# Kernel tuning notes

Hardware: AMD Instinct MI355X
Metric: run time of the kernel (lower is better)

The kernel has to match this reference:

```python
import jax, jax.numpy as jnp
import numpy as np

HID = 128


def _mlp(f, W1, b1, W2, b2, W3, b3):
    h = jax.nn.relu(f @ W1 + b1)
    h = jax.nn.relu(h @ W2 + b2)
    return h @ W3 + b3


def setup_inputs() -> dict:
    key = jax.random.key(0)
    ks = jax.random.split(key, 20)
    B, T = 4096, 256
    x = jax.random.normal(ks[0], (B, T + 1, 2), dtype=jnp.float32)
    t = jax.random.uniform(ks[1], (B, 1), dtype=jnp.float32)

    def lin(k, fan_in, fan_out):
        return jax.random.normal(k, (fan_in, fan_out), jnp.float32) / jnp.sqrt(jnp.float32(fan_in))

    inp = {"x": x, "t": t}
    # forward_score MLP: input = [x_i(2), t(1), x_prev(2), n(1), path_t(2)] = 8
    inp["fw_W1"], inp["fw_b1"] = lin(ks[2], 8, HID), jnp.zeros((HID,), jnp.float32)
    inp["fw_W2"], inp["fw_b2"] = lin(ks[3], HID, HID), jnp.zeros((HID,), jnp.float32)
    inp["fw_W3"], inp["fw_b3"] = lin(ks[4], HID, 2), jnp.zeros((2,), jnp.float32)
    # backward_score MLP: input = [x_i(2), t(1), x_next(2), n(1), path_t(2)] = 8
    inp["bw_W1"], inp["bw_b1"] = lin(ks[5], 8, HID), jnp.zeros((HID,), jnp.float32)
    inp["bw_W2"], inp["bw_b2"] = lin(ks[6], HID, HID), jnp.zeros((HID,), jnp.float32)
    inp["bw_W3"], inp["bw_b3"] = lin(ks[7], HID, 2), jnp.zeros((2,), jnp.float32)
    # initial_score MLP: input = [x_0(2), t(1)] = 3
    inp["in_W1"], inp["in_b1"] = lin(ks[8], 3, HID), jnp.zeros((HID,), jnp.float32)
    inp["in_W2"], inp["in_b2"] = lin(ks[9], HID, HID), jnp.zeros((HID,), jnp.float32)
    inp["in_W3"], inp["in_b3"] = lin(ks[10], HID, 2), jnp.zeros((2,), jnp.float32)
    return inp


def reference(x, t,
              fw_W1, fw_b1, fw_W2, fw_b2, fw_W3, fw_b3,
              bw_W1, bw_b1, bw_W2, bw_b2, bw_W3, bw_b3,
              in_W1, in_b1, in_W2, in_b2, in_W3, in_b3):
    # x: [B, T+1, 2]; last slot is path_t. Equivalent of NeuralNet.get_score,
    # with the per-timestep Python loop batched across the time dimension.
    B = x.shape[0]
    T = x.shape[1] - 1  # ts_len
    x_n = x[:, :-1]                     # [B, T, 2]
    path_t = x[:, -1]                   # [B, 2]

    t_b = jnp.broadcast_to(t[:, None, :], (B, T - 1, 1))        # [B, T-1, 1]
    pt_b = jnp.broadcast_to(path_t[:, None, :], (B, T - 1, 2))  # [B, T-1, 2]

    # forward_score applied at i = 1..T-1, neighbor = x[:, i-1], n = i/T
    n_fwd = (jnp.arange(1, T, dtype=jnp.float32) / T)[None, :, None]
    n_fwd = jnp.broadcast_to(n_fwd, (B, T - 1, 1))
    fwd_feat = jnp.concatenate([x_n[:, 1:], t_b, x_n[:, :-1], n_fwd, pt_b], axis=-1)  # [B,T-1,8]
    fwd_out = _mlp(fwd_feat, fw_W1, fw_b1, fw_W2, fw_b2, fw_W3, fw_b3)                # [B,T-1,2]

    # backward_score applied at i = 0..T-2, neighbor = x[:, i+1], n = i/T
    n_bwd = (jnp.arange(0, T - 1, dtype=jnp.float32) / T)[None, :, None]
    n_bwd = jnp.broadcast_to(n_bwd, (B, T - 1, 1))
    bwd_feat = jnp.concatenate([x_n[:, :-1], t_b, x_n[:, 1:], n_bwd, pt_b], axis=-1)  # [B,T-1,8]
    bwd_out = _mlp(bwd_feat, bw_W1, bw_b1, bw_W2, bw_b2, bw_W3, bw_b3)                # [B,T-1,2]

    # initial_score at i = 0
    init_feat = jnp.concatenate([x_n[:, 0], t], axis=-1)                               # [B,3]
    init_out = _mlp(init_feat, in_W1, in_b1, in_W2, in_b2, in_W3, in_b3)               # [B,2]

    score = jnp.zeros((B, T, 2), dtype=x.dtype)
    score = score.at[:, 1:].add(fwd_out)
    score = score.at[:, :T - 1].add(bwd_out)
    score = score.at[:, 0].add(init_out)
    return score
```

## Files before the change

### kernel.cpp

```cpp
#include <hip/hip_runtime.h>
#include <stdint.h>

typedef __attribute__((ext_vector_type(8))) short short8;
typedef __attribute__((ext_vector_type(4))) float floatx4;

#define MFMA16(a, b, c) __builtin_amdgcn_mfma_f32_16x16x32_bf16(a, b, c, 0, 0, 0)

__device__ __forceinline__ unsigned pkbf(float lo, float hi) {
    const unsigned a = __builtin_bit_cast(unsigned, lo) + 0x8000u;
    const unsigned b = __builtin_bit_cast(unsigned, hi) + 0x8000u;
    return __builtin_amdgcn_perm(b, a, 0x07060302u);
}
__device__ __forceinline__ unsigned short f2bf(float x) {
    unsigned u = __builtin_bit_cast(unsigned, x);
    u = (u + 0x7fffu + ((u >> 16) & 1u)) >> 16;
    return (unsigned short)u;
}

__device__ __forceinline__ int hphys(int row, int u) {
    return row * 64 + ((((u >> 2) ^ (row & 15)) << 2) | (u & 3));
}

__global__ __launch_bounds__(256)
__attribute__((amdgpu_waves_per_eu(4, 4)))
void NeuralNet_37615323578557_kernel(
        const float* __restrict__ x, const float* __restrict__ t,
        const float* __restrict__ fW1, const float* __restrict__ fb1,
        const float* __restrict__ fW2, const float* __restrict__ fb2,
        const float* __restrict__ fW3, const float* __restrict__ fb3,
        const float* __restrict__ gW1, const float* __restrict__ gb1,
        const float* __restrict__ gW2, const float* __restrict__ gb2,
        const float* __restrict__ gW3, const float* __restrict__ gb3,
        const float* __restrict__ iW1, const float* __restrict__ ib1,
        const float* __restrict__ iW2, const float* __restrict__ ib2,
        const float* __restrict__ iW3, const float* __restrict__ ib3,
        float* __restrict__ out) {
    __shared__ unsigned sbuf[8192];
    __shared__ unsigned short fbuf[64 * 8];
    __shared__ float accT[2 * 256 * 2];
    __shared__ unsigned short w3img[256];

    unsigned* const h1buf = sbuf;
    unsigned* const h2buf = sbuf + 4096;

    const int tid  = threadIdx.x;
    const int lane = tid & 63;
    const int w    = tid >> 6;
    const int c    = lane & 15;
    const int q    = lane >> 4;
    const int b0   = blockIdx.x * 2;

    #pragma unroll
    for (int k = 0; k < 4; ++k) accT[tid + k * 256] = 0.0f;
    __syncthreads();

    if (w < 2) {
        float* h1s = (float*)fbuf + w * 128;
        const int b = b0 + w;
        const float* xb = x + (size_t)b * 514;
        const float f0 = xb[0], f1 = xb[1], f2 = t[b];
        const int u0 = lane, u1 = lane + 64;
        const float h0 = fmaxf(iW1[u0] * f0 + iW1[128 + u0] * f1 + iW1[256 + u0] * f2 + ib1[u0], 0.f);
        const float h1 = fmaxf(iW1[u1] * f0 + iW1[128 + u1] * f1 + iW1[256 + u1] * f2 + ib1[u1], 0.f);
        h1s[u0] = h0;
        h1s[u1] = h1;
        float a0 = ib2[lane], a1 = ib2[lane + 64];
        for (int k = 0; k < 128; ++k) {
            const float hv = h1s[k];
            a0 += hv * iW2[k * 128 + lane];
            a1 += hv * iW2[k * 128 + lane + 64];
        }
        a0 = fmaxf(a0, 0.f); a1 = fmaxf(a1, 0.f);
        float p0 = a0 * iW3[lane * 2 + 0] + a1 * iW3[(lane + 64) * 2 + 0];
        float p1 = a0 * iW3[lane * 2 + 1] + a1 * iW3[(lane + 64) * 2 + 1];
        #pragma unroll
        for (int m = 1; m < 64; m <<= 1) {
            p0 += __shfl_xor(p0, m, 64);
            p1 += __shfl_xor(p1, m, 64);
        }
        if (lane == 0) {
            accT[w * 512 + 0] += p0 + ib3[0];
            accT[w * 512 + 1] += p1 + ib3[1];
        }
    }

    const int wbase = w * 32;
    const int ucol  = w * 16 + c;

    for (int dir = 0; dir < 2; ++dir) {
        const float* W1 = dir ? gW1 : fW1;
        const float* B1 = dir ? gb1 : fb1;
        const float* W2 = dir ? gW2 : fW2;
        const float* B2 = dir ? gb2 : fb2;
        const float* W3 = dir ? gW3 : fW3;
        const float* B3 = dir ? gb3 : fb3;
        const int posoff = (1 - dir) * 2;

        __syncthreads();

        {
            const int k0  = (tid & 63) << 1;
            const int c0  = (tid >> 6) << 5;
            const int rot = (tid >> 2) & 15;
            const int ks  = k0 >> 5;
            const int q2  = (k0 >> 3) & 3;
            const int j0  = k0 & 7;
            const float* r0p = &W2[k0 * 128 + c0];
            const float* r1p = r0p + 128;
            const int usb = (q2 << 4) * 8 + j0;
            #pragma unroll 4
            for (int nn2 = 0; nn2 < 16; ++nn2) {
                const int off = ((nn2 + rot) & 15) << 1;
                const float2 v0 = *(const float2*)(r0p + off);
                const float2 v1 = *(const float2*)(r1p + off);
                #pragma unroll
                for (int e = 0; e < 2; ++e) {
                    const int n = c0 + off + e;
                    const unsigned pv = pkbf(e ? v0.y : v0.x, e ? v1.y : v1.x);
                    const int B = ((n >> 5) * 2 + (n & 1)) * 4 + ks;
                    const int us = B * 512 + ((n >> 1) & 15) * 8 + usb;
                    sbuf[us >> 1] = pv;
                }
            }
        }

        if (tid < 128) {
            const int ks3 = tid >> 5, q3 = (tid >> 3) & 3;
            const int c3 = (tid >> 2) & 1, jp = tid & 3;
            const int k = ks3 * 32 + q3 * 8 + jp * 2;
            ((unsigned*)w3img)[tid] = pkbf(W3[k * 2 + c3], W3[(k + 1) * 2 + c3]);
        }

        short8 w1f[2];
        float  b1v[2], b2v[2];
        #pragma unroll
        for (int ntl = 0; ntl < 2; ++ntl) {
            const int col = wbase + 2 * c + ntl;
            b1v[ntl] = B1[col];
            b2v[ntl] = B2[col];
            short8 f = {0, 0, 0, 0, 0, 0, 0, 0};
            if (q == 0) {
                #pragma unroll
                for (int j = 0; j < 8; ++j) f[j] = (short)f2bf(W1[j * 128 + col]);
            }
            w1f[ntl] = f;
        }
        const float b3c = (c < 2) ? B3[c] : 0.0f;
        __syncthreads();

        short8 w2f[2][4];
        {
            const unsigned short* img = (const unsigned short*)sbuf;
            #pragma unroll
            for (int ntl = 0; ntl < 2; ++ntl)
                #pragma unroll
                for (int ks = 0; ks < 4; ++ks)
                    w2f[ntl][ks] = *(const short8*)
                        &img[(((w * 2 + ntl) * 4 + ks) << 9) + lane * 8];
        }

        #pragma unroll 1
        for (int tt = 0; tt < 8; ++tt) {
            const int r0 = tt * 64;

            if (tid < 64) {
                const int r = r0 + tid;
                unsigned v0 = 0, v1 = 0, v2 = 0, v3 = 0;
                if (r < 510) {
                    const int bl = (r >= 255) ? 1 : 0;
                    const int i  = r - bl * 255;
                    const float* xb = x + (size_t)(b0 + bl) * 514;
                    const float2 xi  = *(const float2*)(xb + 2 * i);
                    const float2 xi1 = *(const float2*)(xb + 2 * i + 2);
                    const float2 pt  = *(const float2*)(xb + 512);
                    const float tv = t[b0 + bl];
                    const float nv = (float)(dir ? i : (i + 1)) * (1.0f / 256.0f);
                    if (dir == 0) {
                        v0 = pkbf(xi1.x, xi1.y);
                        v1 = pkbf(tv, xi.x);
                        v2 = pkbf(xi.y, nv);
                    } else {
                        v0 = pkbf(xi.x, xi.y);
                        v1 = pkbf(tv, xi1.x);
                        v2 = pkbf(xi1.y, nv);
                    }
                    v3 = pkbf(pt.x, pt.y);
                }
                unsigned* fp = (unsigned*)&fbuf[tid * 8];
                fp[0] = v0; fp[1] = v1; fp[2] = v2; fp[3] = v3;
            }
            __syncthreads();

            #pragma unroll
            for (int mt = 0; mt < 4; ++mt) {
                short8 af = {0, 0, 0, 0, 0, 0, 0, 0};
                if (q == 0) af = *(const short8*)&fbuf[(mt * 16 + c) * 8];
                floatx4 a0 = {b1v[0], b1v[0], b1v[0], b1v[0]};
                floatx4 a1 = {b1v[1], b1v[1], b1v[1], b1v[1]};
                a0 = MFMA16(af, w1f[0], a0);
                a1 = MFMA16(af, w1f[1], a1);
                const int rowb = mt * 16 + q * 4;
                #pragma unroll
                for (int rr = 0; rr < 4; ++rr)
                    h1buf[hphys(rowb + rr, ucol)] =
                        pkbf(fmaxf(a0[rr], 0.0f), fmaxf(a1[rr], 0.0f));
            }
            __syncthreads();

            #pragma unroll
            for (int mt = 0; mt < 4; ++mt) {
                const unsigned* rp = &h1buf[(mt * 16 + c) * 64];
                const int base = (q ^ c) << 2;
                short8 a0 = *(const short8*)&rp[base];
                short8 a1 = *(const short8*)&rp[base ^ 16];
                short8 a2 = *(const short8*)&rp[base ^ 32];
                short8 a3 = *(const short8*)&rp[base ^ 48];
                floatx4 s0 = {b2v[0], b2v[0], b2v[0], b2v[0]};
                floatx4 s1 = {b2v[1], b2v[1], b2v[1], b2v[1]};
                s0 = MFMA16(a0, w2f[0][0], s0); s1 = MFMA16(a0, w2f[1][0], s1);
                s0 = MFMA16(a1, w2f[0][1], s0); s1 = MFMA16(a1, w2f[1][1], s1);
                s0 = MFMA16(a2, w2f[0][2], s0); s1 = MFMA16(a2, w2f[1][2], s1);
                s0 = MFMA16(a3, w2f[0][3], s0); s1 = MFMA16(a3, w2f[1][3], s1);
                const int rowb = mt * 16 + q * 4;
                #pragma unroll
                for (int rr = 0; rr < 4; ++rr)
                    h2buf[hphys(rowb + rr, ucol)] =
                        pkbf(fmaxf(s0[rr], 0.0f), fmaxf(s1[rr], 0.0f));
            }
            __syncthreads();

            {
                const unsigned* rp = &h2buf[(w * 16 + c) * 64];
                const int base = (q ^ c) << 2;
                short8 a0 = *(const short8*)&rp[base];
                short8 a1 = *(const short8*)&rp[base ^ 16];
                short8 a2 = *(const short8*)&rp[base ^ 32];
                short8 a3 = *(const short8*)&rp[base ^ 48];
                const unsigned short* w3p = w3img + ((q * 2 + (c & 1)) << 3);
                floatx4 s = {b3c, b3c, b3c, b3c};
                s = MFMA16(a0, *(const short8*)&w3p[0],   s);
                s = MFMA16(a1, *(const short8*)&w3p[64],  s);
                s = MFMA16(a2, *(const short8*)&w3p[128], s);
                s = MFMA16(a3, *(const short8*)&w3p[192], s);
                if (c < 2) {
                    const int rb = r0 + w * 16 + q * 4;
                    #pragma unroll
                    for (int rr = 0; rr < 4; ++rr) {
                        const int r = rb + rr;
                        if (r < 510) {
                            const int idx = 2 * r + ((r >= 255) ? 2 : 0)
                                          + posoff + c;
                            atomicAdd(&accT[idx], s[rr]);
                        }
                    }
                }
            }
        }
    }

    __syncthreads();
    ((float4*)(out + (size_t)b0 * 512))[tid] = ((const float4*)accT)[tid];
}

extern "C" void kernel_launch(void* const* d_in, const int* in_sizes, int n_in,
                              void* d_out, int out_size, void* d_ws, size_t ws_size,
                              hipStream_t stream) {
    (void)in_sizes; (void)n_in; (void)d_ws; (void)ws_size; (void)out_size;
    const float* x   = (const float*)d_in[0];
    const float* t   = (const float*)d_in[1];
    const float* fW1 = (const float*)d_in[2];
    const float* fb1 = (const float*)d_in[3];
    const float* fW2 = (const float*)d_in[4];
    const float* fb2 = (const float*)d_in[5];
    const float* fW3 = (const float*)d_in[6];
    const float* fb3 = (const float*)d_in[7];
    const float* gW1 = (const float*)d_in[8];
    const float* gb1 = (const float*)d_in[9];
    const float* gW2 = (const float*)d_in[10];
    const float* gb2 = (const float*)d_in[11];
    const float* gW3 = (const float*)d_in[12];
    const float* gb3 = (const float*)d_in[13];
    const float* iW1 = (const float*)d_in[14];
    const float* ib1 = (const float*)d_in[15];
    const float* iW2 = (const float*)d_in[16];
    const float* ib2 = (const float*)d_in[17];
    const float* iW3 = (const float*)d_in[18];
    const float* ib3 = (const float*)d_in[19];
    float* out = (float*)d_out;

    NeuralNet_37615323578557_kernel<<<dim3(2048), 256, 0, stream>>>(
        x, t, fW1, fb1, fW2, fb2, fW3, fb3,
        gW1, gb1, gW2, gb2, gW3, gb3,
        iW1, ib1, iW2, ib2, iW3, ib3, out);
}
```

Before: 263.4 us.

## Double-buffer feature tiles and overlap next-tile layer-1 with layer-3

Feature staging moves to a double-buffered shared tile that is prefetched two tiles ahead, and the first-layer MFMA for the next tile is computed in the same phase as the current tile's output layer. This removes one block-wide barrier per tile iteration and hides the global loads of x behind compute. It adds a prologue, some extra shared memory, and more complex buffer-reuse ordering.

```diff
diff --git a/kernel.cpp b/kernel.cpp
--- a/kernel.cpp
+++ b/kernel.cpp
@@ -19,6 +19,33 @@
 
 __device__ __forceinline__ int hphys(int row, int u) {
     return row * 64 + ((((u >> 2) ^ (row & 15)) << 2) | (u & 3));
+}
+
+__device__ __forceinline__ void stage_feats(
+        const float* __restrict__ x, const float* __restrict__ t,
+        int b0, int dir, int r, unsigned* fp) {
+    unsigned v0 = 0, v1 = 0, v2 = 0, v3 = 0;
+    if (r < 510) {
+        const int bl = (r >= 255) ? 1 : 0;
+        const int i  = r - bl * 255;
+        const float* xb = x + (size_t)(b0 + bl) * 514;
+        const float2 xi  = *(const float2*)(xb + 2 * i);
+        const float2 xi1 = *(const float2*)(xb + 2 * i + 2);
+        const float2 pt  = *(const float2*)(xb + 512);
+        const float tv = t[b0 + bl];
+        const float nv = (float)(dir ? i : (i + 1)) * (1.0f / 256.0f);
+        if (dir == 0) {
+            v0 = pkbf(xi1.x, xi1.y);
+            v1 = pkbf(tv, xi.x);
+            v2 = pkbf(xi.y, nv);
+        } else {
+            v0 = pkbf(xi.x, xi.y);
+            v1 = pkbf(tv, xi1.x);
+            v2 = pkbf(xi1.y, nv);
+        }
+        v3 = pkbf(pt.x, pt.y);
+    }
+    fp[0] = v0; fp[1] = v1; fp[2] = v2; fp[3] = v3;
 }
 
 __global__ __launch_bounds__(256)
@@ -36,7 +63,7 @@
         const float* __restrict__ iW3, const float* __restrict__ ib3,
         float* __restrict__ out) {
     __shared__ unsigned sbuf[8192];
-    __shared__ unsigned short fbuf[64 * 8];
+    __shared__ unsigned short fbuf[2][64 * 8];
     __shared__ float accT[2 * 256 * 2];
     __shared__ unsigned short w3img[256];
 
@@ -55,7 +82,7 @@
     __syncthreads();
 
     if (w < 2) {
-        float* h1s = (float*)fbuf + w * 128;
+        float* h1s = (float*)&fbuf[0][0] + w * 128;
         const int b = b0 + w;
         const float* xb = x + (size_t)b * 514;
         const float f0 = xb[0], f1 = xb[1], f2 = t[b];
@@ -131,6 +158,10 @@
             ((unsigned*)w3img)[tid] = pkbf(W3[k * 2 + c3], W3[(k + 1) * 2 + c3]);
         }
 
+        if (tid < 128)
+            stage_feats(x, t, b0, dir, tid,
+                        (unsigned*)&fbuf[tid >> 6][(tid & 63) * 8]);
+
         short8 w1f[2];
         float  b1v[2], b2v[2];
         #pragma unroll
@@ -158,54 +189,27 @@
                     w2f[ntl][ks] = *(const short8*)
                         &img[(((w * 2 + ntl) * 4 + ks) << 9) + lane * 8];
         }
+        __syncthreads();
+
+        #pragma unroll
+        for (int mt = 0; mt < 4; ++mt) {
+            short8 af = {0, 0, 0, 0, 0, 0, 0, 0};
+            if (q == 0) af = *(const short8*)&fbuf[0][(mt * 16 + c) * 8];
+            floatx4 a0 = {b1v[0], b1v[0], b1v[0], b1v[0]};
+            floatx4 a1 = {b1v[1], b1v[1], b1v[1], b1v[1]};
+            a0 = MFMA16(af, w1f[0], a0);
+            a1 = MFMA16(af, w1f[1], a1);
+            const int rowb = mt * 16 + q * 4;
+            #pragma unroll
+            for (int rr = 0; rr < 4; ++rr)
+                h1buf[hphys(rowb + rr, ucol)] =
+                    pkbf(fmaxf(a0[rr], 0.0f), fmaxf(a1[rr], 0.0f));
+        }
+        __syncthreads();
 
         #pragma unroll 1
         for (int tt = 0; tt < 8; ++tt) {
             const int r0 = tt * 64;
-
-            if (tid < 64) {
-                const int r = r0 + tid;
-                unsigned v0 = 0, v1 = 0, v2 = 0, v3 = 0;
-                if (r < 510) {
-                    const int bl = (r >= 255) ? 1 : 0;
-                    const int i  = r - bl * 255;
-                    const float* xb = x + (size_t)(b0 + bl) * 514;
-                    const float2 xi  = *(const float2*)(xb + 2 * i);
-                    const float2 xi1 = *(const float2*)(xb + 2 * i + 2);
-                    const float2 pt  = *(const float2*)(xb + 512);
-                    const float tv = t[b0 + bl];
-                    const float nv = (float)(dir ? i : (i + 1)) * (1.0f / 256.0f);
-                    if (dir == 0) {
-                        v0 = pkbf(xi1.x, xi1.y);
-                        v1 = pkbf(tv, xi.x);
-                        v2 = pkbf(xi.y, nv);
-                    } else {
-                        v0 = pkbf(xi.x, xi.y);
-                        v1 = pkbf(tv, xi1.x);
-                        v2 = pkbf(xi1.y, nv);
-                    }
-                    v3 = pkbf(pt.x, pt.y);
-                }
-                unsigned* fp = (unsigned*)&fbuf[tid * 8];
-                fp[0] = v0; fp[1] = v1; fp[2] = v2; fp[3] = v3;
-            }
-            __syncthreads();
-
-            #pragma unroll
-            for (int mt = 0; mt < 4; ++mt) {
-                short8 af = {0, 0, 0, 0, 0, 0, 0, 0};
-                if (q == 0) af = *(const short8*)&fbuf[(mt * 16 + c) * 8];
-                floatx4 a0 = {b1v[0], b1v[0], b1v[0], b1v[0]};
-                floatx4 a1 = {b1v[1], b1v[1], b1v[1], b1v[1]};
-                a0 = MFMA16(af, w1f[0], a0);
-                a1 = MFMA16(af, w1f[1], a1);
-                const int rowb = mt * 16 + q * 4;
-                #pragma unroll
-                for (int rr = 0; rr < 4; ++rr)
-                    h1buf[hphys(rowb + rr, ucol)] =
-                        pkbf(fmaxf(a0[rr], 0.0f), fmaxf(a1[rr], 0.0f));
-            }
-            __syncthreads();
 
             #pragma unroll
             for (int mt = 0; mt < 4; ++mt) {
@@ -230,6 +234,10 @@
             __syncthreads();
 
             {
+                if (tt < 6 && lane < 16)
+                    stage_feats(x, t, b0, dir, (tt + 2) * 64 + w * 16 + lane,
+                                (unsigned*)&fbuf[tt & 1][(w * 16 + lane) * 8]);
+
                 const unsigned* rp = &h2buf[(w * 16 + c) * 64];
                 const int base = (q ^ c) << 2;
                 short8 a0 = *(const short8*)&rp[base];
@@ -254,7 +262,27 @@
                         }
                     }
                 }
+
+                if (tt < 7) {
+                    const unsigned short* ftile = &fbuf[(tt + 1) & 1][0];
+                    #pragma unroll
+                    for (int mt = 0; mt < 4; ++mt) {
+                        short8 af = {0, 0, 0, 0, 0, 0, 0, 0};
+                        if (q == 0)
+                            af = *(const short8*)&ftile[(mt * 16 + c) * 8];
+                        floatx4 a0f = {b1v[0], b1v[0], b1v[0], b1v[0]};
+                        floatx4 a1f = {b1v[1], b1v[1], b1v[1], b1v[1]};
+                        a0f = MFMA16(af, w1f[0], a0f);
+                        a1f = MFMA16(af, w1f[1], a1f);
+                        const int rowb = mt * 16 + q * 4;
+                        #pragma unroll
+                        for (int rr = 0; rr < 4; ++rr)
+                            h1buf[hphys(rowb + rr, ucol)] =
+                                pkbf(fmaxf(a0f[rr], 0.0f), fmaxf(a1f[rr], 0.0f));
+                    }
+                }
             }
+            __syncthreads();
         }
     }
 
```

New measurement: 268.2 us. Within noise of the previous version (+1.8%).
